# Kernel tuning notes

Hardware: AMD Instinct MI355X
Metric: run time of the kernel (lower is better)

## Reference

```python
import jax, jax.numpy as jnp
import numpy as np

K = 4096  # num_embeddings
D = 256   # embedding_dim

def setup_inputs() -> dict:
    key = jax.random.key(0)
    k1, k2 = jax.random.split(key)
    z_e = jax.random.normal(k1, (32, 32, 32, 256), dtype=jnp.float32)
    embedding = jax.random.normal(k2, (K, D), dtype=jnp.float32)
    return {"z_e": z_e, "embedding": embedding}

def reference(z_e, embedding):
    # z_e: [B,H,W,D] channels-last; embedding: [K,D]
    B, H, W, Dd = z_e.shape
    z_flat = z_e.reshape(-1, Dd)                                   # [N,D]
    # squared L2 distances via expansion: ||z||^2 + ||e||^2 - 2 z.e
    distances = (jnp.sum(z_flat**2, axis=1, keepdims=True)
                 + jnp.sum(embedding**2, axis=1)
                 - 2.0 * jnp.matmul(z_flat, embedding.T))          # [N,K]
    indices = jnp.argmin(distances, axis=1)                        # [N]
    z_q = embedding[indices].reshape(B, H, W, Dd)                  # gather
    # straight-through estimator
    z_q = z_e + jax.lax.stop_gradient(z_q - z_e)
    # perplexity (codebook utilization)
    avg_probs = jnp.bincount(indices, length=K).astype(jnp.float32) / indices.shape[0]
    perplexity = jnp.exp(-jnp.sum(avg_probs * jnp.log(avg_probs + 1e-10)))
    return z_q, indices.reshape(B, H, W), perplexity
```

## Files before the change

kernel.cpp:

```cpp
#include <hip/hip_runtime.h>
#include <hip/hip_bf16.h>
#include <math.h>
#include <stdint.h>

typedef _Float16 f16;
typedef _Float16 f16x8 __attribute__((ext_vector_type(8)));
typedef float f32x16 __attribute__((ext_vector_type(16)));

#define DIM 256
#define LOSCALE 2048.0f
#define INV_LOSCALE (1.0f/2048.0f)

#define BP_BYTES (4096u*1024u + 16384u)

#define GLOAD16(gp, lp) __builtin_amdgcn_global_load_lds( \
    (const __attribute__((address_space(1))) void*)(gp),  \
    (__attribute__((address_space(3))) void*)(lp), 16, 0, 0)

__global__ void vq_pack2(const float* __restrict__ emb, f16* __restrict__ bp)
{
    int o = blockIdx.x * blockDim.x + threadIdx.x;
    int l = o & 63;
    int b = o >> 6;
    int t   = b & 1;
    int s   = (b >> 1) & 15;
    int col = b >> 5;
    int code  = col * 32 + (l & 31);
    int depth = s * 16 + (l >> 5) * 8;
    const float* gp = emb + (size_t)code * DIM + depth;
    float4 x0 = *(const float4*)gp;
    float4 x1 = *(const float4*)(gp + 4);
    float xs[8] = {x0.x, x0.y, x0.z, x0.w, x1.x, x1.y, x1.z, x1.w};
    f16x8 v;
    #pragma unroll
    for (int j = 0; j < 8; ++j) {
        f16 h = (f16)xs[j];
        v[j] = t ? (f16)((xs[j] - (float)h) * LOSCALE) : h;
    }
    *(f16x8*)(bp + (size_t)o * 8) = v;
}

__global__ void vq_e2(const float* __restrict__ emb, float* __restrict__ e2) {
    int k = blockIdx.x;
    int l = threadIdx.x;
    float4 v = ((const float4*)(emb + (size_t)k * DIM))[l];
    float s = v.x * v.x + v.y * v.y + v.z * v.z + v.w * v.w;
    #pragma unroll
    for (int off = 32; off; off >>= 1) s += __shfl_xor(s, off);
    if (l == 0) e2[k] = s;
}

__global__ void vq_zero(int* __restrict__ p, int n) {
    int i = blockIdx.x * blockDim.x + threadIdx.x;
    if (i < n) p[i] = 0;
}

__global__ __launch_bounds__(512, 2) void vq_argmin5(
    const float* __restrict__ z, const char* __restrict__ bp,
    const float* __restrict__ e2, float* __restrict__ idxf)
{
    __shared__ __align__(16) char lds[131072];
    __shared__ unsigned long long red[2][4][32];

    const int t    = threadIdx.x;
    const int lane = t & 63;
    const int w    = t >> 6;
    const int rt   = w & 3;
    const int hw   = w >> 2;
    const int l31  = lane & 31;
    const int hi5  = lane >> 5;
    const int rowbase = blockIdx.x * 128 + rt * 32;

    f16x8 a_h[16], a_l[16];
    {
        const float* zr = z + (size_t)(rowbase + l31) * DIM + hi5 * 8;
        #pragma unroll
        for (int s = 0; s < 16; ++s) {
            float4 x0 = *(const float4*)(zr + s * 16);
            float4 x1 = *(const float4*)(zr + s * 16 + 4);
            float xs[8] = {x0.x, x0.y, x0.z, x0.w, x1.x, x1.y, x1.z, x1.w};
            #pragma unroll
            for (int j = 0; j < 8; ++j) {
                f16 h = (f16)xs[j];
                a_h[s][j] = h;
                a_l[s][j] = (f16)((xs[j] - (float)h) * LOSCALE);
            }
        }
    }

    float    bestd[16];
    unsigned bcol[4];
    #pragma unroll
    for (int q = 0; q < 16; ++q) bestd[q] = 3.4e38f;
    #pragma unroll
    for (int i = 0; i < 4; ++i) bcol[i] = 0u;

#define STAGE(pb, cc) do {                                                    \
    const char* src_ = bp + (((size_t)(hw * 64 + (cc))) << 15)                \
                     + (size_t)rt * 8192 + (size_t)lane * 16;                 \
    char* dst_ = lds + (pb) * 65536 + hw * 32768 + rt * 8192;                 \
    _Pragma("unroll")                                                         \
    for (int i_ = 0; i_ < 8; ++i_)                                            \
        GLOAD16(src_ + i_ * 1024, dst_ + i_ * 1024);                          \
    } while (0)

    STAGE(0, 0);
    __syncthreads();
    int cur = 0;

    for (int c = 0; c < 64; ++c) {
        if (c < 63) STAGE(cur ^ 1, c + 1);

        float e2c = e2[hw * 2048 + c * 32 + l31];
        f32x16 acc0, acc1a, acc1b;
        #pragma unroll
        for (int q = 0; q < 16; ++q) { acc0[q] = 0.0f; acc1a[q] = 0.0f; acc1b[q] = 0.0f; }

        const char* bb = lds + cur * 65536 + hw * 32768;
        #pragma unroll
        for (int s = 0; s < 16; ++s) {
            f16x8 bh = *(const f16x8*)(bb + s * 2048 + lane * 16);
            f16x8 bl = *(const f16x8*)(bb + s * 2048 + 1024 + lane * 16);
            acc0  = __builtin_amdgcn_mfma_f32_32x32x16_f16(a_h[s], bh, acc0,  0, 0, 0);
            acc1a = __builtin_amdgcn_mfma_f32_32x32x16_f16(a_h[s], bl, acc1a, 0, 0, 0);
            acc1b = __builtin_amdgcn_mfma_f32_32x32x16_f16(a_l[s], bh, acc1b, 0, 0, 0);
        }

        #pragma unroll
        for (int q = 0; q < 16; ++q) {
            float dot  = fmaf(acc1a[q] + acc1b[q], INV_LOSCALE, acc0[q]);
            float dist = fmaf(-2.0f, dot, e2c);
            bool  lt   = dist < bestd[q];
            bestd[q]   = lt ? dist : bestd[q];
            const unsigned sh = (unsigned)((q & 3) * 8);
            unsigned nv = (bcol[q >> 2] & ~(0xFFu << sh)) | ((unsigned)c << sh);
            bcol[q >> 2] = lt ? nv : bcol[q >> 2];
        }

        __syncthreads();
        cur ^= 1;
    }
#undef STAGE

    #pragma unroll
    for (int q = 0; q < 16; ++q) {
        float    d = bestd[q];
        unsigned c = (unsigned)(hw * 2048) +
                     ((bcol[q >> 2] >> ((q & 3) * 8)) & 0xFFu) * 32u + (unsigned)l31;
        #pragma unroll
        for (int o2 = 16; o2; o2 >>= 1) {
            float    od = __shfl_xor(d, o2);
            unsigned oc = __shfl_xor(c, o2);
            if (od < d || (od == d && oc < c)) { d = od; c = oc; }
        }
        if (l31 == 0) {
            int row = (q & 3) + 8 * (q >> 2) + 4 * hi5;
            unsigned u   = __float_as_uint(d);
            unsigned key = u ^ (unsigned)(((int)u >> 31) | 0x80000000);
            red[hw][rt][row] = ((unsigned long long)key << 32) | c;
        }
    }
    __syncthreads();
    if (t < 128) {
        int rt2 = t >> 5, r = t & 31;
        unsigned long long b0 = red[0][rt2][r];
        unsigned long long b1 = red[1][rt2][r];
        unsigned long long b  = b1 < b0 ? b1 : b0;
        idxf[blockIdx.x * 128 + rt2 * 32 + r] = (float)(unsigned)(b & 0xffffffffu);
    }
}

__global__ __launch_bounds__(256, 2) void vq_argmin_f32(
    const float* __restrict__ z, const float* __restrict__ emb,
    const float* __restrict__ e2, float* __restrict__ idxf, int K)
{
    __shared__ float zs[64 * 36];
    __shared__ float es[128 * 36];
    const int t = threadIdx.x;
    const int tx = t & 15;
    const int ty = t >> 4;
    const int rowbase = blockIdx.x * 64;
    const float* zbase = z + (size_t)rowbase * DIM;
    float best[4]; int bidx[4];
    #pragma unroll
    for (int i = 0; i < 4; ++i) { best[i] = 3.4e38f; bidx[i] = 0; }
    for (int kt = 0; kt < K; kt += 128) {
        float acc[4][8];
        #pragma unroll
        for (int i = 0; i < 4; ++i)
            #pragma unroll
            for (int j = 0; j < 8; ++j) acc[i][j] = 0.0f;
        for (int dc = 0; dc < DIM; dc += 32) {
            { int lr = t >> 2, o = (t & 3) * 8;
              const float* gp = zbase + (size_t)lr * DIM + dc + o;
              *(float4*)&zs[lr*36+o]   = *(const float4*)gp;
              *(float4*)&zs[lr*36+o+4] = *(const float4*)(gp+4); }
            { int lc = t >> 1, o = (t & 1) * 16;
              const float* gp = emb + (size_t)(kt+lc) * DIM + dc + o;
              *(float4*)&es[lc*36+o]    = *(const float4*)gp;
              *(float4*)&es[lc*36+o+4]  = *(const float4*)(gp+4);
              *(float4*)&es[lc*36+o+8]  = *(const float4*)(gp+8);
              *(float4*)&es[lc*36+o+12] = *(const float4*)(gp+12); }
            __syncthreads();
            const float* zp = &zs[(ty*4)*36];
            const float* ep = &es[tx*36];
            #pragma unroll
            for (int d = 0; d < 32; d += 4) {
                float4 zv[4], ev[8];
                #pragma unroll
                for (int i = 0; i < 4; ++i) zv[i] = *(const float4*)&zp[i*36+d];
                #pragma unroll
                for (int j = 0; j < 8; ++j) ev[j] = *(const float4*)&ep[j*16*36+d];
                #pragma unroll
                for (int i = 0; i < 4; ++i)
                    #pragma unroll
                    for (int j = 0; j < 8; ++j) {
                        acc[i][j] += zv[i].x*ev[j].x; acc[i][j] += zv[i].y*ev[j].y;
                        acc[i][j] += zv[i].z*ev[j].z; acc[i][j] += zv[i].w*ev[j].w;
                    }
            }
            __syncthreads();
        }
        #pragma unroll
        for (int j = 0; j < 8; ++j) {
            int c = kt + tx + 16*j;
            float ev2 = e2[c];
            #pragma unroll
            for (int i = 0; i < 4; ++i) {
                float dist = ev2 - 2.0f*acc[i][j];
                if (dist < best[i] || (dist == best[i] && c < bidx[i])) { best[i]=dist; bidx[i]=c; }
            }
        }
    }
    #pragma unroll
    for (int i = 0; i < 4; ++i) {
        float bd = best[i]; int bi = bidx[i];
        #pragma unroll
        for (int off = 8; off; off >>= 1) {
            float od = __shfl_xor(bd, off); int oi = __shfl_xor(bi, off);
            if (od < bd || (od == bd && oi < bi)) { bd = od; bi = oi; }
        }
        if (tx == 0) idxf[rowbase + ty*4 + i] = (float)bi;
    }
}

__global__ void vq_gather(const float* __restrict__ emb,
                          const float* __restrict__ idxf,
                          float* __restrict__ zq, int N)
{
    int n = blockIdx.x * 4 + (threadIdx.x >> 6);
    int l = threadIdx.x & 63;
    if (n >= N) return;
    int idx = (int)idxf[n];
    ((float4*)(zq + (size_t)n * DIM))[l] = ((const float4*)(emb + (size_t)idx * DIM))[l];
}

__global__ void vq_hist(const float* __restrict__ idxf, int* __restrict__ counts, int N) {
    int n = blockIdx.x * blockDim.x + threadIdx.x;
    if (n < N) atomicAdd(&counts[(int)idxf[n]], 1);
}

__global__ void vq_ppl(const int* __restrict__ counts, float invN,
                       float* __restrict__ out, int K)
{
    int t = threadIdx.x;
    float s = 0.0f;
    for (int k = t; k < K; k += 256) {
        float p = (float)counts[k] * invN;
        s += p * logf(p + 1e-10f);
    }
    #pragma unroll
    for (int off = 32; off; off >>= 1) s += __shfl_xor(s, off);
    __shared__ float wsum[4];
    if ((t & 63) == 0) wsum[t >> 6] = s;
    __syncthreads();
    if (t == 0) out[0] = expf(-(wsum[0] + wsum[1] + wsum[2] + wsum[3]));
}

extern "C" void kernel_launch(void* const* d_in, const int* in_sizes, int n_in,
                              void* d_out, int out_size, void* d_ws, size_t ws_size,
                              hipStream_t stream)
{
    const float* z   = (const float*)d_in[0];
    const float* emb = (const float*)d_in[1];
    const int N = in_sizes[0] / DIM;
    const int K = in_sizes[1] / DIM;

    float* out  = (float*)d_out;
    float* zq   = out;
    float* idxf = out + (size_t)N * DIM;
    float* ppl  = idxf + N;

    const size_t NEED = (size_t)BP_BYTES + 16384 + 16384;

    if (ws_size >= NEED && K == 4096 && (N % 128) == 0) {
        f16*   bpk    = (f16*)d_ws;
        float* e2     = (float*)((char*)d_ws + BP_BYTES);
        int*   counts = (int*)((char*)d_ws + BP_BYTES + 16384);

        vq_pack2<<<1024, 256, 0, stream>>>(emb, bpk);
        vq_e2<<<K, 64, 0, stream>>>(emb, e2);
        vq_zero<<<(K + 255) / 256, 256, 0, stream>>>(counts, K);
        vq_argmin5<<<N / 128, 512, 0, stream>>>(z, (const char*)bpk, e2, idxf);
        vq_gather<<<N / 4, 256, 0, stream>>>(emb, idxf, zq, N);
        vq_hist<<<(N + 255) / 256, 256, 0, stream>>>(idxf, counts, N);
        vq_ppl<<<1, 256, 0, stream>>>(counts, 1.0f / (float)N, ppl, K);
    } else {
        float* e2     = (float*)d_ws;
        int*   counts = (int*)((char*)d_ws + (size_t)K * sizeof(float));
        vq_e2<<<K, 64, 0, stream>>>(emb, e2);
        vq_zero<<<(K + 255) / 256, 256, 0, stream>>>(counts, K);
        vq_argmin_f32<<<N / 64, 256, 0, stream>>>(z, emb, e2, idxf, K);
        vq_gather<<<N / 4, 256, 0, stream>>>(emb, idxf, zq, N);
        vq_hist<<<(N + 255) / 256, 256, 0, stream>>>(idxf, counts, N);
        vq_ppl<<<1, 256, 0, stream>>>(counts, 1.0f / (float)N, ppl, K);
    }
}
```

Before: 241.3 us.

## Split argmin into per-codebook-half blocks with global partial combine

The 512-thread block that handled both codebook halves is split into two 256-thread blocks, each scanning one half of the codebook with its own 64KB double-buffered LDS. Partial minima go to a workspace buffer and a new combine kernel reduces them, replacing the in-block LDS reduction. This aims to improve occupancy and scheduling flexibility with smaller blocks and less LDS per block. It also adds s_setprio around the MFMA loop. The costs are an extra kernel launch, a global round trip for the partials, and a fast path now restricted to N == 32768.

```diff
diff --git a/kernel.cpp b/kernel.cpp
--- a/kernel.cpp
+++ b/kernel.cpp
@@ -55,21 +55,20 @@
     if (i < n) p[i] = 0;
 }
 
-__global__ __launch_bounds__(512, 2) void vq_argmin5(
+__global__ __launch_bounds__(256, 2) void vq_argmin6(
     const float* __restrict__ z, const char* __restrict__ bp,
-    const float* __restrict__ e2, float* __restrict__ idxf)
-{
-    __shared__ __align__(16) char lds[131072];
-    __shared__ unsigned long long red[2][4][32];
+    const float* __restrict__ e2, unsigned long long* __restrict__ part)
+{
+    __shared__ __align__(16) char lds[2][32768];
 
     const int t    = threadIdx.x;
     const int lane = t & 63;
-    const int w    = t >> 6;
-    const int rt   = w & 3;
-    const int hw   = w >> 2;
+    const int rt   = t >> 6;
+    const int hw   = blockIdx.x & 1;
+    const int rg   = blockIdx.x >> 1;
     const int l31  = lane & 31;
     const int hi5  = lane >> 5;
-    const int rowbase = blockIdx.x * 128 + rt * 32;
+    const int rowbase = rg * 128 + rt * 32;
 
     f16x8 a_h[16], a_l[16];
     {
@@ -95,13 +94,14 @@
     #pragma unroll
     for (int i = 0; i < 4; ++i) bcol[i] = 0u;
 
+    const char* bhalf = bp + ((size_t)hw << 21);
+
 #define STAGE(pb, cc) do {                                                    \
-    const char* src_ = bp + (((size_t)(hw * 64 + (cc))) << 15)                \
-                     + (size_t)rt * 8192 + (size_t)lane * 16;                 \
-    char* dst_ = lds + (pb) * 65536 + hw * 32768 + rt * 8192;                 \
+    const char* src_ = bhalf + ((size_t)(cc) << 15) + (size_t)t * 16;         \
+    char* dst_ = lds[pb] + t * 16;                                            \
     _Pragma("unroll")                                                         \
     for (int i_ = 0; i_ < 8; ++i_)                                            \
-        GLOAD16(src_ + i_ * 1024, dst_ + i_ * 1024);                          \
+        GLOAD16(src_ + i_ * 4096, dst_ + i_ * 4096);                          \
     } while (0)
 
     STAGE(0, 0);
@@ -116,7 +116,8 @@
         #pragma unroll
         for (int q = 0; q < 16; ++q) { acc0[q] = 0.0f; acc1a[q] = 0.0f; acc1b[q] = 0.0f; }
 
-        const char* bb = lds + cur * 65536 + hw * 32768;
+        const char* bb = lds[cur];
+        __builtin_amdgcn_s_setprio(1);
         #pragma unroll
         for (int s = 0; s < 16; ++s) {
             f16x8 bh = *(const f16x8*)(bb + s * 2048 + lane * 16);
@@ -125,6 +126,7 @@
             acc1a = __builtin_amdgcn_mfma_f32_32x32x16_f16(a_h[s], bl, acc1a, 0, 0, 0);
             acc1b = __builtin_amdgcn_mfma_f32_32x32x16_f16(a_l[s], bh, acc1b, 0, 0, 0);
         }
+        __builtin_amdgcn_s_setprio(0);
 
         #pragma unroll
         for (int q = 0; q < 16; ++q) {
@@ -157,17 +159,21 @@
             int row = (q & 3) + 8 * (q >> 2) + 4 * hi5;
             unsigned u   = __float_as_uint(d);
             unsigned key = u ^ (unsigned)(((int)u >> 31) | 0x80000000);
-            red[hw][rt][row] = ((unsigned long long)key << 32) | c;
-        }
-    }
-    __syncthreads();
-    if (t < 128) {
-        int rt2 = t >> 5, r = t & 31;
-        unsigned long long b0 = red[0][rt2][r];
-        unsigned long long b1 = red[1][rt2][r];
-        unsigned long long b  = b1 < b0 ? b1 : b0;
-        idxf[blockIdx.x * 128 + rt2 * 32 + r] = (float)(unsigned)(b & 0xffffffffu);
-    }
+            part[(size_t)hw * 32768 + rowbase + row] =
+                ((unsigned long long)key << 32) | c;
+        }
+    }
+}
+
+__global__ void vq_combine(const unsigned long long* __restrict__ part,
+                           float* __restrict__ idxf, int N)
+{
+    int i = blockIdx.x * blockDim.x + threadIdx.x;
+    if (i >= N) return;
+    unsigned long long a = part[i];
+    unsigned long long b = part[(size_t)N + i];
+    unsigned long long m = b < a ? b : a;
+    idxf[i] = (float)(unsigned)(m & 0xffffffffu);
 }
 
 __global__ __launch_bounds__(256, 2) void vq_argmin_f32(
@@ -291,17 +297,21 @@
     float* idxf = out + (size_t)N * DIM;
     float* ppl  = idxf + N;
 
-    const size_t NEED = (size_t)BP_BYTES + 16384 + 16384;
-
-    if (ws_size >= NEED && K == 4096 && (N % 128) == 0) {
+    const size_t PART_BYTES = 2ull * 32768 * sizeof(unsigned long long);
+    const size_t NEED = (size_t)BP_BYTES + 16384 + 16384 + PART_BYTES;
+
+    if (ws_size >= NEED && K == 4096 && N == 32768) {
         f16*   bpk    = (f16*)d_ws;
         float* e2     = (float*)((char*)d_ws + BP_BYTES);
         int*   counts = (int*)((char*)d_ws + BP_BYTES + 16384);
+        unsigned long long* part =
+            (unsigned long long*)((char*)d_ws + BP_BYTES + 32768);
 
         vq_pack2<<<1024, 256, 0, stream>>>(emb, bpk);
         vq_e2<<<K, 64, 0, stream>>>(emb, e2);
         vq_zero<<<(K + 255) / 256, 256, 0, stream>>>(counts, K);
-        vq_argmin5<<<N / 128, 512, 0, stream>>>(z, (const char*)bpk, e2, idxf);
+        vq_argmin6<<<(N / 128) * 2, 256, 0, stream>>>(z, (const char*)bpk, e2, part);
+        vq_combine<<<N / 256, 256, 0, stream>>>(part, idxf, N);
         vq_gather<<<N / 4, 256, 0, stream>>>(emb, idxf, zq, N);
         vq_hist<<<(N + 255) / 256, 256, 0, stream>>>(idxf, counts, N);
         vq_ppl<<<1, 256, 0, stream>>>(counts, 1.0f / (float)N, ppl, K);
```

Result: no change. 242.7 us (+0.6%).
